# Optimization experiments

Hardware: AMD Instinct MI355X
Metric: run time of the kernel (lower is better)

The kernel has to match this reference:

```python
import jax, jax.numpy as jnp
import numpy as np

TAU = 2.0        # LIFNode tau
ALPHA = 4.0      # spikingjelly default surrogate Sigmoid alpha
EPS = 1e-5       # BatchNorm eps
NUM_HEADS = 8

@jax.custom_vjp
def spike(u):
    # Heaviside with sigmoid surrogate gradient (spikingjelly default)
    return (u >= 0.0).astype(u.dtype)

def _spike_fwd(u):
    return spike(u), u

def _spike_bwd(u, g):
    s = jax.nn.sigmoid(ALPHA * u)
    return (g * ALPHA * s * (1.0 - s),)

spike.defvjp(_spike_fwd, _spike_bwd)

def lif(x, vth=1.0):
    # single-step LIF from rest (v=0, v_reset=0, decay_input=True): v = x / tau
    return spike(x / TAU - vth)

def conv1x1_bn(x, w, gamma, beta, mean, var):
    # 1x1 conv (no bias) + eval-mode BatchNorm, fused affine
    y = jnp.einsum('oc,bchw->bohw', w, x)
    inv = gamma / jnp.sqrt(var + EPS)
    return y * inv[None, :, None, None] + (beta - mean * inv)[None, :, None, None]


def setup_inputs() -> dict:
    B, C, H, W = 16, 768, 32, 32
    key = jax.random.key(0)
    ks = jax.random.split(key, 22)
    def bn(i):
        return (jax.random.uniform(ks[i], (C,)) + 0.5,
                0.1 * jax.random.normal(ks[i + 1], (C,)),
                0.1 * jax.random.normal(ks[i + 2], (C,)),
                jax.random.uniform(ks[i + 3], (C,)) + 0.5)
    q_gamma, q_beta, q_mean, q_var = bn(1)
    k_gamma, k_beta, k_mean, k_var = bn(5)
    v_gamma, v_beta, v_mean, v_var = bn(9)
    p_gamma, p_beta, p_mean, p_var = bn(13)
    W_SCALE = 0.25  # keeps post-BN activations spanning the LIF threshold
    return {
        'x': 3.0 * jax.random.normal(ks[0], (B, C, H, W), dtype=jnp.float32),
        'wq': W_SCALE * jax.random.normal(ks[17], (C, C), dtype=jnp.float32),
        'q_gamma': q_gamma, 'q_beta': q_beta, 'q_mean': q_mean, 'q_var': q_var,
        'wk': W_SCALE * jax.random.normal(ks[18], (C, C), dtype=jnp.float32),
        'k_gamma': k_gamma, 'k_beta': k_beta, 'k_mean': k_mean, 'k_var': k_var,
        'wv': W_SCALE * jax.random.normal(ks[19], (C, C), dtype=jnp.float32),
        'v_gamma': v_gamma, 'v_beta': v_beta, 'v_mean': v_mean, 'v_var': v_var,
        'wp': W_SCALE * jax.random.normal(ks[20], (C, C), dtype=jnp.float32),
        'bp': 0.1 * jax.random.normal(ks[21], (C,), dtype=jnp.float32),
        'p_gamma': p_gamma, 'p_beta': p_beta, 'p_mean': p_mean, 'p_var': p_var,
    }


def reference(x, wq, q_gamma, q_beta, q_mean, q_var,
              wk, k_gamma, k_beta, k_mean, k_var,
              wv, v_gamma, v_beta, v_mean, v_var,
              wp, bp, p_gamma, p_beta, p_mean, p_var):
    B, C, H, W = x.shape
    N = H * W
    h = NUM_HEADS
    hd = C // h
    identity = x
    xs = lif(x)  # shortcut_lif

    def branch(w, g, b, m, vv):
        y = lif(conv1x1_bn(xs, w, g, b, m, vv))            # [B,C,H,W] binary spikes
        y = y.reshape(B, C, N).transpose(0, 2, 1)           # [B,N,C]
        return y.reshape(B, N, h, hd).transpose(0, 2, 1, 3)  # [B,h,N,hd]

    q = branch(wq, q_gamma, q_beta, q_mean, q_var)
    k = branch(wk, k_gamma, k_beta, k_mean, k_var)
    v = branch(wv, v_gamma, v_beta, v_mean, v_var)

    kv = jnp.sum(k * v, axis=2, keepdims=True)  # [B,h,1,hd] token reduction
    kv = lif(kv, vth=0.5)                       # attn_lif

    out = q * kv                                          # [B,h,N,hd]
    out = out.transpose(0, 2, 1, 3).reshape(B, N, C)      # [B,N,C]
    out = out.transpose(0, 2, 1).reshape(B, C, H, W)      # [B,C,H,W]

    y = jnp.einsum('oc,bchw->bohw', wp, out) + bp[None, :, None, None]
    inv = p_gamma / jnp.sqrt(p_var + EPS)
    y = y * inv[None, :, None, None] + (p_beta - p_mean * inv)[None, :, None, None]
    return y + identity
```

## Files before the change

kernel.cpp:

```cpp
#include <hip/hip_runtime.h>
#include <cstdint>
#include <cstddef>

#define C_DIM 768
#define NPIX  1024
#define B_DIM 16
#define NTOT  16384
#define KT_N  12
#define MT_N  6
#define JT_N  128
#define MT2_N 12
#define TAU   2.0e-3f
#define BCAP  64
#define NBLK  (3 * MT2_N * JT_N)
#define PLANE_B (C_DIM * C_DIM)
#define TILE_B  8192

typedef __attribute__((ext_vector_type(4)))  int   int4v;
typedef __attribute__((ext_vector_type(16))) char  char16v;

__device__ __forceinline__ void gload16(const void* g, void* l) {
    __builtin_amdgcn_global_load_lds(
        (const __attribute__((address_space(1))) unsigned int*)g,
        (__attribute__((address_space(3))) unsigned int*)l, 16, 0, 0);
}

__global__ __launch_bounds__(256) void prep_weights(
    const float* __restrict__ w0, const float* __restrict__ w1,
    const float* __restrict__ w2, const float* __restrict__ w3,
    char* __restrict__ wall)
{
    const int tile = blockIdx.x;
    const int set  = blockIdx.y;
    const int kt = tile / MT_N, mt = tile % MT_N;
    const float* w = set == 0 ? w0 : set == 1 ? w1 : set == 2 ? w2 : w3;
    char* pl = wall + (size_t)set * 2 * PLANE_B;
#pragma unroll
    for (int i = 0; i < 2; ++i) {
        int q = threadIdx.x + i * 256;
        int kg = q >> 7, m = q & 127;
        int o = mt * 128 + m;
        int cbase = kt * 64 + kg * 16;
        char16v H, L;
#pragma unroll
        for (int e = 0; e < 16; ++e) {
            float wv = w[(size_t)o * C_DIM + cbase + e];
            int w16 = (int)lrintf(wv * 16384.0f);
            w16 = w16 > 32639 ? 32639 : (w16 < -32639 ? -32639 : w16);
            int hi = (w16 + 128) >> 8;
            int lo = w16 - (hi << 8);
            H[e] = (char)hi;
            L[e] = (char)lo;
        }
        size_t base = (size_t)tile * TILE_B + (size_t)q * 16;
        *(char16v*)(pl + base)           = H;
        *(char16v*)(pl + PLANE_B + base) = L;
    }
}

__global__ __launch_bounds__(256) void prep_bn(
    const float* __restrict__ qg, const float* __restrict__ qb,
    const float* __restrict__ qm, const float* __restrict__ qv,
    const float* __restrict__ kg, const float* __restrict__ kb,
    const float* __restrict__ km, const float* __restrict__ kv,
    const float* __restrict__ vg, const float* __restrict__ vb,
    const float* __restrict__ vm, const float* __restrict__ vv,
    const float* __restrict__ pg, const float* __restrict__ pb,
    const float* __restrict__ pm, const float* __restrict__ pv,
    float* __restrict__ invt, float* __restrict__ biast)
{
    int i = blockIdx.x * 256 + threadIdx.x;
    if (i >= 4 * C_DIM) return;
    int set = i / C_DIM, o = i - set * C_DIM;
    const float* g = set == 0 ? qg : set == 1 ? kg : set == 2 ? vg : pg;
    const float* b = set == 0 ? qb : set == 1 ? kb : set == 2 ? vb : pb;
    const float* m = set == 0 ? qm : set == 1 ? km : set == 2 ? vm : pm;
    const float* v = set == 0 ? qv : set == 1 ? kv : set == 2 ? vv : pv;
    float inv = g[o] / sqrtf(v[o] + 1e-5f);
    invt[i]  = inv;
    biast[i] = b[o] - m[o] * inv;
}

__global__ __launch_bounds__(256) void prep_spikes(
    const float* __restrict__ x, char* __restrict__ xs)
{
    const int jt = blockIdx.x;
    const int kt = blockIdx.y;
    const int b  = jt >> 3;
    const int n0 = (jt & 7) * 128;
#pragma unroll
    for (int i = 0; i < 2; ++i) {
        int q = threadIdx.x + i * 256;
        int kg = q >> 7, col = q & 127;
        char16v sv;
#pragma unroll
        for (int e = 0; e < 16; ++e) {
            float xv = x[((size_t)b * C_DIM + (kt * 64 + kg * 16 + e)) * NPIX + n0 + col];
            sv[e] = (xv >= 2.0f) ? (char)1 : (char)0;
        }
        *(char16v*)(xs + (size_t)(jt * KT_N + kt) * TILE_B + (size_t)q * 16) = sv;
    }
}

__global__ __launch_bounds__(256, 4) void branch_mfma(
    const char* __restrict__ wall, const char* __restrict__ xsblob,
    const float* __restrict__ invt, const float* __restrict__ biast,
    char* __restrict__ sall,
    unsigned int* __restrict__ cntArr, unsigned int* __restrict__ recsB)
{
    __shared__ char stage[2][16384];
    __shared__ unsigned int lcnt;
    const int jt = blockIdx.x, mt = blockIdx.y, z = blockIdx.z;
    const int tid = threadIdx.x;
    const int lane = tid & 63, wid = tid >> 6;
    const int wm = wid >> 1, wn = wid & 1;
    const int lr = lane & 15, kg = lane >> 4;
    const char* wblob = wall + (size_t)z * 2 * PLANE_B;
    char* sblob = sall + (size_t)z * (size_t)C_DIM * NTOT;
    const float* invz  = invt  + z * C_DIM;
    const float* biasz = biast + z * C_DIM;
    const unsigned int blk = ((unsigned)z * MT2_N + mt) * JT_N + jt;

    const int s_kg = tid >> 6, s_m = tid & 63;
    const int mt128 = mt >> 1, mrow = (mt & 1) * 64;

#define STG(buf, ktA) do {                                                     \
        const char* Ab_ = wblob + (size_t)((ktA) * MT_N + mt128) * TILE_B;     \
        const char* Bb_ = xsblob + (size_t)(jt * KT_N + (ktA)) * TILE_B;       \
        char* d_ = stage[buf];                                                 \
        gload16(Ab_ + s_kg * 2048 + (size_t)(mrow + s_m) * 16,                 \
                d_ + s_kg * 1024 + s_m * 16);                                  \
        gload16(Ab_ + PLANE_B + s_kg * 2048 + (size_t)(mrow + s_m) * 16,       \
                d_ + 4096 + s_kg * 1024 + s_m * 16);                           \
        gload16(Bb_ + (size_t)tid * 16,        d_ + 8192 + tid * 16);          \
        gload16(Bb_ + 4096 + (size_t)tid * 16, d_ + 12288 + tid * 16);         \
    } while (0)

    int4v acch[2][4], accl[2][4];
#pragma unroll
    for (int a = 0; a < 2; ++a)
#pragma unroll
        for (int b2 = 0; b2 < 4; ++b2) {
            acch[a][b2] = (int4v){0, 0, 0, 0};
            accl[a][b2] = (int4v){0, 0, 0, 0};
        }

    STG(0, 0);
    STG(1, 1);
    if (tid == 0) lcnt = 0;
    int cur = 0;
    const int arow = (wm * 32 + lr) * 16;
    for (int kt = 0; kt < KT_N; ++kt) {
        if (kt + 1 < KT_N) asm volatile("s_waitcnt vmcnt(4)");
        else               asm volatile("s_waitcnt vmcnt(0)");
        __builtin_amdgcn_s_barrier();
        __builtin_amdgcn_sched_barrier(0);
        const char* st = stage[cur];
        int4v ah0 = *(const int4v*)&st[kg * 1024 + arow];
        int4v ah1 = *(const int4v*)&st[kg * 1024 + arow + 256];
        int4v al0 = *(const int4v*)&st[4096 + kg * 1024 + arow];
        int4v al1 = *(const int4v*)&st[4096 + kg * 1024 + arow + 256];
        int4v bfr[4];
#pragma unroll
        for (int fn = 0; fn < 4; ++fn)
            bfr[fn] = *(const int4v*)&st[8192 + kg * 2048 + (wn * 64 + fn * 16 + lr) * 16];
        __builtin_amdgcn_sched_barrier(0);
        asm volatile("s_waitcnt lgkmcnt(0)");
        __builtin_amdgcn_sched_barrier(0);
        __builtin_amdgcn_s_barrier();
        if (kt + 2 < KT_N) STG(cur, kt + 2);
        __builtin_amdgcn_s_setprio(1);
#pragma unroll
        for (int fn = 0; fn < 4; ++fn) {
            acch[0][fn] = __builtin_amdgcn_mfma_i32_16x16x64_i8(ah0, bfr[fn], acch[0][fn], 0, 0, 0);
            acch[1][fn] = __builtin_amdgcn_mfma_i32_16x16x64_i8(ah1, bfr[fn], acch[1][fn], 0, 0, 0);
            accl[0][fn] = __builtin_amdgcn_mfma_i32_16x16x64_i8(al0, bfr[fn], accl[0][fn], 0, 0, 0);
            accl[1][fn] = __builtin_amdgcn_mfma_i32_16x16x64_i8(al1, bfr[fn], accl[1][fn], 0, 0, 0);
        }
        __builtin_amdgcn_s_setprio(0);
        cur ^= 1;
    }
#undef STG

    unsigned int pk[2][4];
#pragma unroll
    for (int fm = 0; fm < 2; ++fm)
#pragma unroll
        for (int fn = 0; fn < 4; ++fn) {
            unsigned int p = 0;
#pragma unroll
            for (int r = 0; r < 4; ++r) {
                int o = mt * 64 + wm * 32 + fm * 16 + kg * 4 + r;
                int vi = acch[fm][fn][r] * 256 + accl[fm][fn][r];
                float y = (float)vi * 6.103515625e-05f;
                float ybn = y * invz[o] + biasz[o];
                if (ybn >= 2.0f) p |= (1u << (r * 8));
                if (fabsf(ybn - 2.0f) < TAU) {
                    unsigned int idx = atomicAdd(&lcnt, 1u);
                    if (idx < BCAP) {
                        int j = jt * 128 + wn * 64 + fn * 16 + lr;
                        recsB[(size_t)blk * BCAP + idx] =
                            ((unsigned)z << 24) | ((unsigned)o << 14) | (unsigned)j;
                    }
                }
            }
            pk[fm][fn] = p;
        }

#pragma unroll
    for (int fnPair = 0; fnPair < 2; ++fnPair) {
        unsigned int got[4];
#pragma unroll
        for (int t = 0; t < 4; ++t) {
            int sel = (kg + t) & 3;
            int sfm = sel >> 1, sfn = (sel & 1) * 2 + fnPair;
            unsigned int send =
                sfm == 0 ? (sfn == 0 ? pk[0][0] : sfn == 1 ? pk[0][1] : sfn == 2 ? pk[0][2] : pk[0][3])
                         : (sfn == 0 ? pk[1][0] : sfn == 1 ? pk[1][1] : sfn == 2 ? pk[1][2] : pk[1][3]);
            int src = (((kg - t) & 3) << 4) + lr;
            got[t] = (unsigned int)__shfl((int)send, src);
        }
        unsigned int part[4];
#pragma unroll
        for (int j = 0; j < 4; ++j) {
            int tsel = (kg - j) & 3;
            part[j] = tsel == 0 ? got[0] : tsel == 1 ? got[1]
                    : tsel == 2 ? got[2] : got[3];
        }
        int4v chunk = (int4v){(int)part[0], (int)part[1], (int)part[2], (int)part[3]};
        int kg2 = wm * 2 + (kg >> 1);
        int col = wn * 64 + ((kg & 1) * 2 + fnPair) * 16 + lr;
        size_t off = (size_t)(jt * KT_N + mt) * TILE_B + (size_t)kg2 * 2048 + (size_t)col * 16;
        *(int4v*)(sblob + off) = chunk;
    }
    __syncthreads();
    if (tid == 0) {
        unsigned int c = lcnt;
        cntArr[blk] = c > BCAP ? BCAP : c;
    }
}

__global__ __launch_bounds__(256) void fixup(
    const char* __restrict__ xs,
    const float* __restrict__ wq, const float* __restrict__ wk, const float* __restrict__ wv,
    const float* __restrict__ qg, const float* __restrict__ qb, const float* __restrict__ qm, const float* __restrict__ qv,
    const float* __restrict__ kg, const float* __restrict__ kb2, const float* __restrict__ km, const float* __restrict__ kvr,
    const float* __restrict__ vg, const float* __restrict__ vb, const float* __restrict__ vm, const float* __restrict__ vv,
    char* __restrict__ sq, char* __restrict__ sk, char* __restrict__ sv,
    const unsigned int* __restrict__ cntArr, const unsigned int* __restrict__ recsB)
{
#pragma clang fp contract(off)
    __shared__ float cw[4][C_DIM];
    const int lane = threadIdx.x & 63;
    const int wvid = threadIdx.x >> 6;
    const int gwave = blockIdx.x * 4 + wvid;
    const int nwaves = gridDim.x * 4;
    const int npairs = NBLK * BCAP;

    for (int p = gwave; p < npairs; p += nwaves) {
        int slot = p / NBLK;
        int reg  = p - slot * NBLK;
        if ((unsigned)slot >= cntArr[reg]) continue;
        unsigned int rec = recsB[(size_t)reg * BCAP + slot];
        int plane = rec >> 24, o = (rec >> 14) & 1023, j = rec & 16383;
        int jt = j >> 7, col = j & 127;
        const float* w = plane == 0 ? wq : plane == 1 ? wk : wv;
        int base = 0;
#pragma unroll
        for (int cc = 0; cc < 12; ++cc) {
            int c = cc * 64 + lane;
            char s = xs[(size_t)(jt * KT_N + (c >> 6)) * TILE_B
                        + ((c >> 4) & 3) * 2048 + col * 16 + (c & 15)];
            float wvv = w[(size_t)o * C_DIM + c];
            bool act = (s != 0);
            unsigned long long m = __ballot(act);
            int pos = __popcll(m & ((1ull << lane) - 1ull));
            if (act) cw[wvid][base + pos] = wvv;
            base += __popcll(m);
        }
        __builtin_amdgcn_s_waitcnt(0);
        if (lane == 0) {
            float s = 0.0f;
            for (int i = 0; i < base; ++i) s = s + cw[wvid][i];
            const float* g  = plane == 0 ? qg : plane == 1 ? kg : vg;
            const float* be = plane == 0 ? qb : plane == 1 ? kb2 : vb;
            const float* me = plane == 0 ? qm : plane == 1 ? km : vm;
            const float* va = plane == 0 ? qv : plane == 1 ? kvr : vv;
            float invv = g[o] / sqrtf(va[o] + 1e-5f);
            float t1 = me[o] * invv;
            float bias = be[o] - t1;
            float t3 = s * invv;
            float ybn = t3 + bias;
            char spv = (ybn >= 2.0f) ? (char)1 : (char)0;
            char* blob = plane == 0 ? sq : plane == 1 ? sk : sv;
            blob[(size_t)(jt * KT_N + (o >> 6)) * TILE_B
                 + ((o >> 4) & 3) * 2048 + col * 16 + (o & 15)] = spv;
        }
    }
}

__global__ __launch_bounds__(256) void kv_mask_blob(
    const char* __restrict__ sk, const char* __restrict__ sv,
    unsigned char* __restrict__ maskb)
{
    const int kt = blockIdx.x, b = blockIdx.y;
    const int t = threadIdx.x;
    const int kg = t >> 6;
    const int col0 = (t & 63) * 2;
    __shared__ unsigned int lmask[4][4];
    if (t < 16) lmask[t >> 2][t & 3] = 0;
    __syncthreads();
    uint4 acc = make_uint4(0, 0, 0, 0);
    for (int jti = 0; jti < 8; ++jti) {
        size_t base = (size_t)((b * 8 + jti) * KT_N + kt) * TILE_B + kg * 2048;
#pragma unroll
        for (int cc = 0; cc < 2; ++cc) {
            uint4 kk = *(const uint4*)(sk + base + (size_t)(col0 + cc) * 16);
            uint4 vv = *(const uint4*)(sv + base + (size_t)(col0 + cc) * 16);
            acc.x |= (kk.x & vv.x); acc.y |= (kk.y & vv.y);
            acc.z |= (kk.z & vv.z); acc.w |= (kk.w & vv.w);
        }
    }
    if (acc.x) atomicOr(&lmask[kg][0], acc.x);
    if (acc.y) atomicOr(&lmask[kg][1], acc.y);
    if (acc.z) atomicOr(&lmask[kg][2], acc.z);
    if (acc.w) atomicOr(&lmask[kg][3], acc.w);
    __syncthreads();
    if (t < 64) {
        int kg2 = t >> 4, e = t & 15;
        unsigned int dw = lmask[kg2][e >> 2];
        unsigned char byte = (dw >> ((e & 3) * 8)) & 0xFF;
        maskb[(size_t)b * C_DIM + kt * 64 + t] = byte ? 1 : 0;
    }
}

__global__ __launch_bounds__(256, 4) void final_mfma(
    const char* __restrict__ wblob, const char* __restrict__ sqblob,
    const unsigned char* __restrict__ maskb,
    const float* __restrict__ x, const float* __restrict__ bp,
    const float* __restrict__ invt, const float* __restrict__ biast,
    float* __restrict__ out)
{
    __shared__ char stage[2][16384];
    __shared__ char mlds[768];
    const int jt = blockIdx.x, mt = blockIdx.y;
    const int tid = threadIdx.x;
    const int lane = tid & 63, wid = tid >> 6;
    const int wm = wid >> 1, wn = wid & 1;
    const int lr = lane & 15, kg = lane >> 4;
    const int b = jt >> 3;
    const float* invp  = invt  + 3 * C_DIM;
    const float* biasp = biast + 3 * C_DIM;

    const int s_kg = tid >> 6, s_m = tid & 63;
    const int mt128 = mt >> 1, mrow = (mt & 1) * 64;

#define STG(buf, ktA) do {                                                     \
        const char* Ab_ = wblob + (size_t)((ktA) * MT_N + mt128) * TILE_B;     \
        const char* Bb_ = sqblob + (size_t)(jt * KT_N + (ktA)) * TILE_B;       \
        char* d_ = stage[buf];                                                 \
        gload16(Ab_ + s_kg * 2048 + (size_t)(mrow + s_m) * 16,                 \
                d_ + s_kg * 1024 + s_m * 16);                                  \
        gload16(Ab_ + PLANE_B + s_kg * 2048 + (size_t)(mrow + s_m) * 16,       \
                d_ + 4096 + s_kg * 1024 + s_m * 16);                           \
        gload16(Bb_ + (size_t)tid * 16,        d_ + 8192 + tid * 16);          \
        gload16(Bb_ + 4096 + (size_t)tid * 16, d_ + 12288 + tid * 16);         \
    } while (0)

    int4v acch[2][4], accl[2][4];
#pragma unroll
    for (int a = 0; a < 2; ++a)
#pragma unroll
        for (int b2 = 0; b2 < 4; ++b2) {
            acch[a][b2] = (int4v){0, 0, 0, 0};
            accl[a][b2] = (int4v){0, 0, 0, 0};
        }

    if (tid < 48)
        *(int4v*)&mlds[tid * 16] = *(const int4v*)(maskb + (size_t)b * C_DIM + tid * 16);
    STG(0, 0);
    STG(1, 1);
    __syncthreads();
    int cur = 0;
    const int arow = (wm * 32 + lr) * 16;
    for (int kt = 0; kt < KT_N; ++kt) {
        if (kt + 1 < KT_N) asm volatile("s_waitcnt vmcnt(4)");
        else               asm volatile("s_waitcnt vmcnt(0)");
        __builtin_amdgcn_s_barrier();
        __builtin_amdgcn_sched_barrier(0);
        const char* st = stage[cur];
        int4v ah0 = *(const int4v*)&st[kg * 1024 + arow];
        int4v ah1 = *(const int4v*)&st[kg * 1024 + arow + 256];
        int4v al0 = *(const int4v*)&st[4096 + kg * 1024 + arow];
        int4v al1 = *(const int4v*)&st[4096 + kg * 1024 + arow + 256];
        int4v mp = *(const int4v*)&mlds[kt * 64 + kg * 16];
        int4v bfr[4];
#pragma unroll
        for (int fn = 0; fn < 4; ++fn)
            bfr[fn] = *(const int4v*)&st[8192 + kg * 2048 + (wn * 64 + fn * 16 + lr) * 16];
        __builtin_amdgcn_sched_barrier(0);
        asm volatile("s_waitcnt lgkmcnt(0)");
        __builtin_amdgcn_sched_barrier(0);
        __builtin_amdgcn_s_barrier();
        if (kt + 2 < KT_N) STG(cur, kt + 2);
#pragma unroll
        for (int fn = 0; fn < 4; ++fn) bfr[fn] &= mp;
        __builtin_amdgcn_s_setprio(1);
#pragma unroll
        for (int fn = 0; fn < 4; ++fn) {
            acch[0][fn] = __builtin_amdgcn_mfma_i32_16x16x64_i8(ah0, bfr[fn], acch[0][fn], 0, 0, 0);
            acch[1][fn] = __builtin_amdgcn_mfma_i32_16x16x64_i8(ah1, bfr[fn], acch[1][fn], 0, 0, 0);
            accl[0][fn] = __builtin_amdgcn_mfma_i32_16x16x64_i8(al0, bfr[fn], accl[0][fn], 0, 0, 0);
            accl[1][fn] = __builtin_amdgcn_mfma_i32_16x16x64_i8(al1, bfr[fn], accl[1][fn], 0, 0, 0);
        }
        __builtin_amdgcn_s_setprio(0);
        cur ^= 1;
    }
#undef STG

    const int n0 = (jt & 7) * 128;
#pragma unroll
    for (int fm = 0; fm < 2; ++fm)
#pragma unroll
        for (int fn = 0; fn < 4; ++fn)
#pragma unroll
            for (int r = 0; r < 4; ++r) {
                int p = mt * 64 + wm * 32 + fm * 16 + kg * 4 + r;
                int nl = wn * 64 + fn * 16 + lr;
                int vi = acch[fm][fn][r] * 256 + accl[fm][fn][r];
                float pre = (float)vi * 6.103515625e-05f;
                size_t idx = ((size_t)b * C_DIM + p) * NPIX + n0 + nl;
                out[idx] = (pre + bp[p]) * invp[p] + biasp[p] + x[idx];
            }
}

extern "C" void kernel_launch(void* const* d_in, const int* in_sizes, int n_in,
                              void* d_out, int out_size, void* d_ws, size_t ws_size,
                              hipStream_t stream) {
    const float* x  = (const float*)d_in[0];
    const float* wq = (const float*)d_in[1];
    const float* qg = (const float*)d_in[2];
    const float* qb = (const float*)d_in[3];
    const float* qm = (const float*)d_in[4];
    const float* qv = (const float*)d_in[5];
    const float* wk = (const float*)d_in[6];
    const float* kg = (const float*)d_in[7];
    const float* kb = (const float*)d_in[8];
    const float* km = (const float*)d_in[9];
    const float* kvv= (const float*)d_in[10];
    const float* wv = (const float*)d_in[11];
    const float* vg = (const float*)d_in[12];
    const float* vb = (const float*)d_in[13];
    const float* vm = (const float*)d_in[14];
    const float* vv = (const float*)d_in[15];
    const float* wp = (const float*)d_in[16];
    const float* bp = (const float*)d_in[17];
    const float* pg = (const float*)d_in[18];
    const float* pb = (const float*)d_in[19];
    const float* pm = (const float*)d_in[20];
    const float* pv = (const float*)d_in[21];

    const size_t SPIKE = (size_t)C_DIM * NTOT;
    char* sq  = (char*)d_ws;
    char* sk  = sq + SPIKE;
    char* sv  = sk + SPIKE;
    char* xs  = sv + SPIKE;
    char* wall = xs + SPIKE;
    unsigned char* maskb = (unsigned char*)(wall + (size_t)4 * 2 * PLANE_B);
    unsigned int* cntArr = (unsigned int*)(maskb + 16384);
    unsigned int* recsB  = cntArr + NBLK;
    float* invt  = (float*)(recsB + (size_t)NBLK * BCAP);
    float* biast = invt + 4 * C_DIM;
    char* wpb = wall + (size_t)3 * 2 * PLANE_B;

    prep_weights<<<dim3(KT_N * MT_N, 4), 256, 0, stream>>>(wq, wk, wv, wp, wall);
    prep_bn<<<12, 256, 0, stream>>>(qg, qb, qm, qv, kg, kb, km, kvv,
                                    vg, vb, vm, vv, pg, pb, pm, pv, invt, biast);
    prep_spikes<<<dim3(JT_N, KT_N), 256, 0, stream>>>(x, xs);
    branch_mfma<<<dim3(JT_N, MT2_N, 3), 256, 0, stream>>>(
        wall, xs, invt, biast, sq, cntArr, recsB);
    fixup<<<2048, 256, 0, stream>>>(xs, wq, wk, wv,
                                    qg, qb, qm, qv, kg, kb, km, kvv, vg, vb, vm, vv,
                                    sq, sk, sv, cntArr, recsB);
    kv_mask_blob<<<dim3(KT_N, B_DIM), 256, 0, stream>>>(sk, sv, maskb);
    final_mfma<<<dim3(JT_N, MT2_N), 256, 0, stream>>>(
        wpb, sq, maskb, x, bp, invt, biast, (float*)d_out);
}
```

Before: 159.8 us.

## Widen MFMA block tiles to two column tiles sharing each weight stage

Both branch_mfma and final_mfma now run 512-thread blocks that each cover two adjacent 128-column spike tiles. The weight A-tile is staged once in shared memory and read by eight waves instead of four, which halves the A-side global and LDS staging traffic per output and halves the block count. The cost is larger shared-memory stages (24KB per buffer), fewer blocks in flight, and heavier barriers across eight waves. The per-block cancellation-record capacity (BCAP) now covers twice as many outputs.

```diff
diff --git a/kernel.cpp b/kernel.cpp
--- a/kernel.cpp
+++ b/kernel.cpp
@@ -9,10 +9,11 @@
 #define KT_N  12
 #define MT_N  6
 #define JT_N  128
+#define JT2_N 64
 #define MT2_N 12
 #define TAU   2.0e-3f
 #define BCAP  64
-#define NBLK  (3 * MT2_N * JT_N)
+#define NBLK  (3 * MT2_N * JT2_N)
 #define PLANE_B (C_DIM * C_DIM)
 #define TILE_B  8192
 
@@ -102,38 +103,39 @@
     }
 }
 
-__global__ __launch_bounds__(256, 4) void branch_mfma(
+__global__ __launch_bounds__(512, 4) void branch_mfma(
     const char* __restrict__ wall, const char* __restrict__ xsblob,
     const float* __restrict__ invt, const float* __restrict__ biast,
     char* __restrict__ sall,
     unsigned int* __restrict__ cntArr, unsigned int* __restrict__ recsB)
 {
-    __shared__ char stage[2][16384];
+    __shared__ char stage[2][24576];
     __shared__ unsigned int lcnt;
-    const int jt = blockIdx.x, mt = blockIdx.y, z = blockIdx.z;
+    const int jt2 = blockIdx.x, mt = blockIdx.y, z = blockIdx.z;
+    const int jt0 = jt2 * 2;
     const int tid = threadIdx.x;
     const int lane = tid & 63, wid = tid >> 6;
-    const int wm = wid >> 1, wn = wid & 1;
+    const int wm = wid >> 2, wn = wid & 3;
     const int lr = lane & 15, kg = lane >> 4;
     const char* wblob = wall + (size_t)z * 2 * PLANE_B;
     char* sblob = sall + (size_t)z * (size_t)C_DIM * NTOT;
     const float* invz  = invt  + z * C_DIM;
     const float* biasz = biast + z * C_DIM;
-    const unsigned int blk = ((unsigned)z * MT2_N + mt) * JT_N + jt;
-
-    const int s_kg = tid >> 6, s_m = tid & 63;
+    const unsigned int blk = ((unsigned)z * MT2_N + mt) * JT2_N + jt2;
+
     const int mt128 = mt >> 1, mrow = (mt & 1) * 64;
+    const int aIdx = tid & 255;
+    const size_t aoff_src = (size_t)((tid < 256) ? 0 : PLANE_B)
+                          + (aIdx >> 6) * 2048 + (size_t)(mrow + (aIdx & 63)) * 16;
 
 #define STG(buf, ktA) do {                                                     \
         const char* Ab_ = wblob + (size_t)((ktA) * MT_N + mt128) * TILE_B;     \
-        const char* Bb_ = xsblob + (size_t)(jt * KT_N + (ktA)) * TILE_B;       \
+        const char* B0_ = xsblob + (size_t)(jt0 * KT_N + (ktA)) * TILE_B;      \
+        const char* B1_ = xsblob + (size_t)((jt0 + 1) * KT_N + (ktA)) * TILE_B;\
         char* d_ = stage[buf];                                                 \
-        gload16(Ab_ + s_kg * 2048 + (size_t)(mrow + s_m) * 16,                 \
-                d_ + s_kg * 1024 + s_m * 16);                                  \
-        gload16(Ab_ + PLANE_B + s_kg * 2048 + (size_t)(mrow + s_m) * 16,       \
-                d_ + 4096 + s_kg * 1024 + s_m * 16);                           \
-        gload16(Bb_ + (size_t)tid * 16,        d_ + 8192 + tid * 16);          \
-        gload16(Bb_ + 4096 + (size_t)tid * 16, d_ + 12288 + tid * 16);         \
+        gload16(Ab_ + aoff_src,                d_ + tid * 16);                 \
+        gload16(B0_ + (size_t)tid * 16,        d_ + 8192 + tid * 16);          \
+        gload16(B1_ + (size_t)tid * 16,        d_ + 16384 + tid * 16);         \
     } while (0)
 
     int4v acch[2][4], accl[2][4];
@@ -150,8 +152,9 @@
     if (tid == 0) lcnt = 0;
     int cur = 0;
     const int arow = (wm * 32 + lr) * 16;
+    const int bbase = 8192 + (wn >> 1) * 8192 + ((wn & 1) * 64) * 16;
     for (int kt = 0; kt < KT_N; ++kt) {
-        if (kt + 1 < KT_N) asm volatile("s_waitcnt vmcnt(4)");
+        if (kt + 1 < KT_N) asm volatile("s_waitcnt vmcnt(3)");
         else               asm volatile("s_waitcnt vmcnt(0)");
         __builtin_amdgcn_s_barrier();
         __builtin_amdgcn_sched_barrier(0);
@@ -163,7 +166,7 @@
         int4v bfr[4];
 #pragma unroll
         for (int fn = 0; fn < 4; ++fn)
-            bfr[fn] = *(const int4v*)&st[8192 + kg * 2048 + (wn * 64 + fn * 16 + lr) * 16];
+            bfr[fn] = *(const int4v*)&st[bbase + kg * 2048 + (fn * 16 + lr) * 16];
         __builtin_amdgcn_sched_barrier(0);
         asm volatile("s_waitcnt lgkmcnt(0)");
         __builtin_amdgcn_sched_barrier(0);
@@ -182,6 +185,8 @@
     }
 #undef STG
 
+    const int jtw = jt0 + (wn >> 1);
+    const int colb = (wn & 1) * 64;
     unsigned int pk[2][4];
 #pragma unroll
     for (int fm = 0; fm < 2; ++fm)
@@ -198,7 +203,7 @@
                 if (fabsf(ybn - 2.0f) < TAU) {
                     unsigned int idx = atomicAdd(&lcnt, 1u);
                     if (idx < BCAP) {
-                        int j = jt * 128 + wn * 64 + fn * 16 + lr;
+                        int j = jtw * 128 + colb + fn * 16 + lr;
                         recsB[(size_t)blk * BCAP + idx] =
                             ((unsigned)z << 24) | ((unsigned)o << 14) | (unsigned)j;
                     }
@@ -229,8 +234,8 @@
         }
         int4v chunk = (int4v){(int)part[0], (int)part[1], (int)part[2], (int)part[3]};
         int kg2 = wm * 2 + (kg >> 1);
-        int col = wn * 64 + ((kg & 1) * 2 + fnPair) * 16 + lr;
-        size_t off = (size_t)(jt * KT_N + mt) * TILE_B + (size_t)kg2 * 2048 + (size_t)col * 16;
+        int col = colb + ((kg & 1) * 2 + fnPair) * 16 + lr;
+        size_t off = (size_t)(jtw * KT_N + mt) * TILE_B + (size_t)kg2 * 2048 + (size_t)col * 16;
         *(int4v*)(sblob + off) = chunk;
     }
     __syncthreads();
@@ -334,37 +339,38 @@
     }
 }
 
-__global__ __launch_bounds__(256, 4) void final_mfma(
+__global__ __launch_bounds__(512, 4) void final_mfma(
     const char* __restrict__ wblob, const char* __restrict__ sqblob,
     const unsigned char* __restrict__ maskb,
     const float* __restrict__ x, const float* __restrict__ bp,
     const float* __restrict__ invt, const float* __restrict__ biast,
     float* __restrict__ out)
 {
-    __shared__ char stage[2][16384];
+    __shared__ char stage[2][24576];
     __shared__ char mlds[768];
-    const int jt = blockIdx.x, mt = blockIdx.y;
+    const int jt2 = blockIdx.x, mt = blockIdx.y;
+    const int jt0 = jt2 * 2;
     const int tid = threadIdx.x;
     const int lane = tid & 63, wid = tid >> 6;
-    const int wm = wid >> 1, wn = wid & 1;
+    const int wm = wid >> 2, wn = wid & 3;
     const int lr = lane & 15, kg = lane >> 4;
-    const int b = jt >> 3;
+    const int b = jt0 >> 3;
     const float* invp  = invt  + 3 * C_DIM;
     const float* biasp = biast + 3 * C_DIM;
 
-    const int s_kg = tid >> 6, s_m = tid & 63;
     const int mt128 = mt >> 1, mrow = (mt & 1) * 64;
+    const int aIdx = tid & 255;
+    const size_t aoff_src = (size_t)((tid < 256) ? 0 : PLANE_B)
+                          + (aIdx >> 6) * 2048 + (size_t)(mrow + (aIdx & 63)) * 16;
 
 #define STG(buf, ktA) do {                                                     \
         const char* Ab_ = wblob + (size_t)((ktA) * MT_N + mt128) * TILE_B;     \
-        const char* Bb_ = sqblob + (size_t)(jt * KT_N + (ktA)) * TILE_B;       \
+        const char* B0_ = sqblob + (size_t)(jt0 * KT_N + (ktA)) * TILE_B;      \
+        const char* B1_ = sqblob + (size_t)((jt0 + 1) * KT_N + (ktA)) * TILE_B;\
         char* d_ = stage[buf];                                                 \
-        gload16(Ab_ + s_kg * 2048 + (size_t)(mrow + s_m) * 16,                 \
-                d_ + s_kg * 1024 + s_m * 16);                                  \
-        gload16(Ab_ + PLANE_B + s_kg * 2048 + (size_t)(mrow + s_m) * 16,       \
-                d_ + 4096 + s_kg * 1024 + s_m * 16);                           \
-        gload16(Bb_ + (size_t)tid * 16,        d_ + 8192 + tid * 16);          \
-        gload16(Bb_ + 4096 + (size_t)tid * 16, d_ + 12288 + tid * 16);         \
+        gload16(Ab_ + aoff_src,                d_ + tid * 16);                 \
+        gload16(B0_ + (size_t)tid * 16,        d_ + 8192 + tid * 16);          \
+        gload16(B1_ + (size_t)tid * 16,        d_ + 16384 + tid * 16);         \
     } while (0)
 
     int4v acch[2][4], accl[2][4];
@@ -383,8 +389,9 @@
     __syncthreads();
     int cur = 0;
     const int arow = (wm * 32 + lr) * 16;
+    const int bbase = 8192 + (wn >> 1) * 8192 + ((wn & 1) * 64) * 16;
     for (int kt = 0; kt < KT_N; ++kt) {
-        if (kt + 1 < KT_N) asm volatile("s_waitcnt vmcnt(4)");
+        if (kt + 1 < KT_N) asm volatile("s_waitcnt vmcnt(3)");
         else               asm volatile("s_waitcnt vmcnt(0)");
         __builtin_amdgcn_s_barrier();
         __builtin_amdgcn_sched_barrier(0);
@@ -397,7 +404,7 @@
         int4v bfr[4];
 #pragma unroll
         for (int fn = 0; fn < 4; ++fn)
-            bfr[fn] = *(const int4v*)&st[8192 + kg * 2048 + (wn * 64 + fn * 16 + lr) * 16];
+            bfr[fn] = *(const int4v*)&st[bbase + kg * 2048 + (fn * 16 + lr) * 16];
         __builtin_amdgcn_sched_barrier(0);
         asm volatile("s_waitcnt lgkmcnt(0)");
         __builtin_amdgcn_sched_barrier(0);
@@ -418,7 +425,9 @@
     }
 #undef STG
 
-    const int n0 = (jt & 7) * 128;
+    const int jtw = jt0 + (wn >> 1);
+    const int n0 = (jtw & 7) * 128;
+    const int colb = (wn & 1) * 64;
 #pragma unroll
     for (int fm = 0; fm < 2; ++fm)
 #pragma unroll
@@ -426,7 +435,7 @@
 #pragma unroll
             for (int r = 0; r < 4; ++r) {
                 int p = mt * 64 + wm * 32 + fm * 16 + kg * 4 + r;
-                int nl = wn * 64 + fn * 16 + lr;
+                int nl = colb + fn * 16 + lr;
                 int vi = acch[fm][fn][r] * 256 + accl[fm][fn][r];
                 float pre = (float)vi * 6.103515625e-05f;
                 size_t idx = ((size_t)b * C_DIM + p) * NPIX + n0 + nl;
@@ -477,12 +486,12 @@
     prep_bn<<<12, 256, 0, stream>>>(qg, qb, qm, qv, kg, kb, km, kvv,
                                     vg, vb, vm, vv, pg, pb, pm, pv, invt, biast);
     prep_spikes<<<dim3(JT_N, KT_N), 256, 0, stream>>>(x, xs);
-    branch_mfma<<<dim3(JT_N, MT2_N, 3), 256, 0, stream>>>(
+    branch_mfma<<<dim3(JT2_N, MT2_N, 3), 512, 0, stream>>>(
         wall, xs, invt, biast, sq, cntArr, recsB);
     fixup<<<2048, 256, 0, stream>>>(xs, wq, wk, wv,
                                     qg, qb, qm, qv, kg, kb, km, kvv, vg, vb, vm, vv,
                                     sq, sk, sv, cntArr, recsB);
     kv_mask_blob<<<dim3(KT_N, B_DIM), 256, 0, stream>>>(sk, sv, maskb);
-    final_mfma<<<dim3(JT_N, MT2_N), 256, 0, stream>>>(
+    final_mfma<<<dim3(JT2_N, MT2_N), 512, 0, stream>>>(
         wpb, sq, maskb, x, bp, invt, biast, (float*)d_out);
 }
```

After: 153.5 us. 4.0% less time.
